# Kernel optimization log

Hardware: AMD Instinct MI355X
Metric: run time of the kernel (lower is better)

## Reference

```python
import jax, jax.numpy as jnp
import numpy as np
from jax import lax

K = 3
PAD = 1
STRIDE = 1


def setup_inputs() -> dict:
    key = jax.random.key(0)
    k1, k2, k3 = jax.random.split(key, 3)
    B, Cin, Cout, H, W = 4, 64, 64, 128, 128
    x = jax.random.normal(k1, (B, Cin, H, W), dtype=jnp.float32)
    # offset-generating conv weight: [2*K*K, Cin, K, K]
    w_offset = jax.random.normal(k2, (2 * K * K, Cin, K, K), dtype=jnp.float32) * 0.05
    # deformable conv weight: [Cout, Cin, K, K]
    w_deform = jax.random.normal(k3, (Cout, Cin, K, K), dtype=jnp.float32) * 0.05
    return {"x": x, "w_offset": w_offset, "w_deform": w_deform}


def _bilinear_sample_one(img, ys, xs):
    # img: [C, H, W]; ys, xs: [K2, Ho, Wo] float sampling coords
    H, W = img.shape[1], img.shape[2]
    y0 = jnp.floor(ys)
    x0 = jnp.floor(xs)
    wy = ys - y0  # frac weights, [K2, Ho, Wo]
    wx = xs - x0

    def gather(yi, xi):
        valid = (yi >= 0) & (yi <= H - 1) & (xi >= 0) & (xi <= W - 1)
        yc = jnp.clip(yi, 0, H - 1).astype(jnp.int32)
        xc = jnp.clip(xi, 0, W - 1).astype(jnp.int32)
        # img[:, yc, xc] -> [C, K2, Ho, Wo]; zero outside (torchvision zero-pad)
        return img[:, yc, xc] * valid[None].astype(img.dtype)

    v00 = gather(y0, x0)
    v01 = gather(y0, x0 + 1)
    v10 = gather(y0 + 1, x0)
    v11 = gather(y0 + 1, x0 + 1)
    w00 = ((1 - wy) * (1 - wx))[None]
    w01 = ((1 - wy) * wx)[None]
    w10 = (wy * (1 - wx))[None]
    w11 = (wy * wx)[None]
    return v00 * w00 + v01 * w01 + v10 * w10 + v11 * w11  # [C, K2, Ho, Wo]


def reference(x, w_offset, w_deform):
    B, Cin, H, W = x.shape
    Cout = w_deform.shape[0]
    K2 = K * K
    # 1) plain conv to produce offsets: [B, 2*K2, H, W]
    offset = lax.conv_general_dilated(
        x, w_offset, window_strides=(STRIDE, STRIDE),
        padding=((PAD, PAD), (PAD, PAD)),
        dimension_numbers=("NCHW", "OIHW", "NCHW"))
    Ho, Wo = offset.shape[2], offset.shape[3]
    # torchvision ordering: channel 2*k = dy, 2*k+1 = dx, taps row-major
    off = offset.reshape(B, K2, 2, Ho, Wo)
    dy, dx = off[:, :, 0], off[:, :, 1]  # [B, K2, Ho, Wo]
    # 2) base sampling grid per kernel tap
    kk = jnp.arange(K2)
    ki = (kk // K).astype(jnp.float32)  # tap row
    kj = (kk % K).astype(jnp.float32)   # tap col
    base_y = (jnp.arange(Ho, dtype=jnp.float32) * STRIDE - PAD)[None, :] + ki[:, None]  # [K2, Ho]
    base_x = (jnp.arange(Wo, dtype=jnp.float32) * STRIDE - PAD)[None, :] + kj[:, None]  # [K2, Wo]
    ys = base_y[None, :, :, None] + dy  # [B, K2, Ho, Wo]
    xs = base_x[None, :, None, :] + dx
    # 3) deformable bilinear gather: [B, Cin, K2, Ho, Wo]
    sampled = jax.vmap(_bilinear_sample_one)(x, ys, xs)
    # 4) weighted accumulation (the conv contraction)
    out = jnp.einsum("ock,bckhw->bohw", w_deform.reshape(Cout, Cin, K2), sampled)
    return out
```

## Files before the change

### kernel.cpp

```cpp
#include <hip/hip_runtime.h>


#define BATCH 4
#define CIN   64
#define COUT  64
#define HH    128
#define WW    128
#define HWPIX (HH*WW)

typedef __attribute__((ext_vector_type(8))) short short8;
typedef __attribute__((ext_vector_type(4))) float floatx4;

__device__ __forceinline__ unsigned short f2bf(float f) {
  unsigned int u = __float_as_uint(f);
  unsigned int r = u + 0x7fffu + ((u >> 16) & 1u);
  return (unsigned short)(r >> 16);
}
__device__ __forceinline__ float bf2f(unsigned short h) { return __uint_as_float(((unsigned int)h) << 16); }
__device__ __forceinline__ float lo16f(unsigned int u) { return __uint_as_float(u << 16); }
__device__ __forceinline__ float hi16f(unsigned int u) { return __uint_as_float(u & 0xffff0000u); }

__device__ __forceinline__ unsigned int bilin2(unsigned int u00, unsigned int u01,
                                               unsigned int u10, unsigned int u11,
                                               float w00, float w01, float w10, float w11) {
  float lo = w00 * lo16f(u00) + w01 * lo16f(u01) + w10 * lo16f(u10) + w11 * lo16f(u11);
  float hi = w00 * hi16f(u00) + w01 * hi16f(u01) + w10 * hi16f(u10) + w11 * hi16f(u11);
  unsigned int r;
  asm("v_cvt_pk_bf16_f32 %0, %1, %2" : "=v"(r) : "v"(lo), "v"(hi));
  return r;
}

__device__ __forceinline__ int swz(int a) { return a ^ (((a >> 9) & 3) << 4); }

__global__ __launch_bounds__(256) void pre_kernel(const float* __restrict__ x,
                                                  const float* __restrict__ wo,
                                                  const float* __restrict__ wd,
                                                  unsigned short* __restrict__ xThi,
                                                  unsigned short* __restrict__ xTlo,
                                                  unsigned short* __restrict__ wdA,
                                                  unsigned short* __restrict__ woAhi,
                                                  unsigned short* __restrict__ woAlo) {
  int tid = threadIdx.x;
  if (blockIdx.x < 4096) {
    __shared__ float tile[32][33];
    int t = blockIdx.x;
    int b = t >> 10, rem = t & 1023;
    int c0 = (rem >> 9) * 32, p0 = (rem & 511) * 32;
    int tx = tid & 31, ty = tid >> 5;
    const float* xb = x + (size_t)b * CIN * HWPIX;
    size_t boff = (size_t)b * HWPIX * CIN;
#pragma unroll
    for (int i = 0; i < 4; i++)
      tile[ty + i * 8][tx] = xb[(size_t)(c0 + ty + i * 8) * HWPIX + p0 + tx];
    __syncthreads();
#pragma unroll
    for (int i = 0; i < 2; i++) {
      int tt = tid + i * 256;
      int row = tt >> 4;
      int cp = tt & 15;
      float v0 = tile[cp * 2][row], v1 = tile[cp * 2 + 1][row];
      unsigned short h0 = f2bf(v0), h1 = f2bf(v1);
      unsigned short l0 = f2bf(v0 - bf2f(h0)), l1 = f2bf(v1 - bf2f(h1));
      size_t o = boff + (size_t)(p0 + row) * CIN + c0 + cp * 2;
      *(ushort2*)&xThi[o] = make_ushort2(h0, h1);
      *(ushort2*)&xTlo[o] = make_ushort2(l0, l1);
    }
  } else {
    int t = (blockIdx.x - 4096) * 256 + tid;
    if (t < 36864) {
      int j = t & 7, lane = (t >> 3) & 63, ct = (t >> 9) & 3, kc = (t >> 11) & 1, kk = t >> 12;
      int cout = ct * 16 + (lane & 15);
      int cin  = kc * 32 + (lane >> 4) * 8 + j;
      wdA[t] = f2bf(wd[(size_t)(cout * CIN + cin) * 9 + kk]);
    }
    int t2 = t - 36864;
    if (t2 >= 0 && t2 < 18432) {
      int j = t2 & 7, lane = (t2 >> 3) & 63, ct = (t2 >> 9) & 1, kc = (t2 >> 10) & 1, kk = t2 >> 11;
      int cout = ct * 16 + (lane & 15);
      int cin  = kc * 32 + (lane >> 4) * 8 + j;
      float v = (cout < 18) ? wo[(size_t)(cout * CIN + cin) * 9 + kk] : 0.f;
      unsigned short h = f2bf(v);
      woAhi[t2] = h;
      woAlo[t2] = f2bf(v - bf2f(h));
    }
  }
}

__global__ __launch_bounds__(256) void fused_dcn_kernel(const unsigned short* __restrict__ xThi,
                                                        const unsigned short* __restrict__ xTlo,
                                                        const unsigned short* __restrict__ woAhi,
                                                        const unsigned short* __restrict__ woAlo,
                                                        const unsigned short* __restrict__ wdA,
                                                        float* __restrict__ out) {
  __shared__ unsigned short sBhi2[2][4096];
  __shared__ unsigned short sBlo2[2][4096];
  __shared__ float offL[18 * 64];
  char* sHc = (char*)sBhi2;
  char* sLc = (char*)sBlo2;

  int tid = threadIdx.x;
  int hw = blockIdx.x;
  int bid = (hw & 7) * 128 + (hw >> 3);
  int b = bid >> 8, r = bid & 255, y = r >> 1, x0 = (r & 1) << 6;

  int p1 = tid >> 2, si = tid & 3;
  int lane = tid & 63, w = tid >> 6;

  const unsigned short* xhib = xThi + (size_t)b * HWPIX * CIN;
  const unsigned short* xlob = xTlo + (size_t)b * HWPIX * CIN;

  int wq = p1 >> 4, iq = p1 & 15;
  int kcd = si >> 1, qb = si & 1;
  int wb0 = ((((wq * 2 + kcd) * 64) + qb * 32 + iq) * 8) * 2;
  int wb1 = wb0 + 256;
  int swb0 = swz(wb0), swb1 = swz(wb1);
  int brb0[4], brb1[4];
#pragma unroll
  for (int pg = 0; pg < 4; pg++) {
    brb0[pg] = swz(pg * 2048 + lane * 16);
    brb1[pg] = swz(pg * 2048 + 1024 + lane * 16);
  }

  int xp = x0 + p1;

  floatx4 oacc[2];
  oacc[0] = (floatx4){0.f, 0.f, 0.f, 0.f};
  oacc[1] = (floatx4){0.f, 0.f, 0.f, 0.f};
  int ctA = w & 1, pgA = (w >> 1) * 2;

  auto ldA = [&](int kk, uint4& h0, uint4& h1, uint4& l0, uint4& l1) {
    int ys = y - 1 + kk / 3;
    int xs = xp - 1 + kk % 3;
    bool valid = (ys >= 0) && (ys < HH) && (xs >= 0) && (xs < WW);
    h0 = (uint4){0, 0, 0, 0}; h1 = h0; l0 = h0; l1 = h0;
    if (valid) {
      const unsigned short* ph = xhib + (size_t)(ys * WW + xs) * CIN + si * 16;
      const unsigned short* pl = xlob + (size_t)(ys * WW + xs) * CIN + si * 16;
      h0 = *(const uint4*)ph; h1 = *(const uint4*)(ph + 8);
      l0 = *(const uint4*)pl; l1 = *(const uint4*)(pl + 8);
    }
  };
  auto stageA = [&](int nxt, const uint4& h0, const uint4& h1, const uint4& l0, const uint4& l1) {
    *(uint4*)(sHc + nxt * 8192 + swb0) = h0;
    *(uint4*)(sHc + nxt * 8192 + swb1) = h1;
    *(uint4*)(sLc + nxt * 8192 + swb0) = l0;
    *(uint4*)(sLc + nxt * 8192 + swb1) = l1;
  };
  auto mfmaA = [&](int kk, int cur) {
    const short8* Ah = (const short8*)(woAhi + (size_t)kk * 2048);
    const short8* Al = (const short8*)(woAlo + (size_t)kk * 2048);
    short8 ah0 = Ah[ctA * 64 + lane], ah1 = Ah[128 + ctA * 64 + lane];
    short8 al0 = Al[ctA * 64 + lane], al1 = Al[128 + ctA * 64 + lane];
#pragma unroll
    for (int pgi = 0; pgi < 2; pgi++) {
      int pg = pgA + pgi;
      short8 bh0 = *(const short8*)(sHc + cur * 8192 + brb0[pg]);
      short8 bh1 = *(const short8*)(sHc + cur * 8192 + brb1[pg]);
      short8 bl0 = *(const short8*)(sLc + cur * 8192 + brb0[pg]);
      short8 bl1 = *(const short8*)(sLc + cur * 8192 + brb1[pg]);
      oacc[pgi] = __builtin_amdgcn_mfma_f32_16x16x32_bf16(ah0, bh0, oacc[pgi], 0, 0, 0);
      oacc[pgi] = __builtin_amdgcn_mfma_f32_16x16x32_bf16(ah0, bl0, oacc[pgi], 0, 0, 0);
      oacc[pgi] = __builtin_amdgcn_mfma_f32_16x16x32_bf16(al0, bh0, oacc[pgi], 0, 0, 0);
      oacc[pgi] = __builtin_amdgcn_mfma_f32_16x16x32_bf16(ah1, bh1, oacc[pgi], 0, 0, 0);
      oacc[pgi] = __builtin_amdgcn_mfma_f32_16x16x32_bf16(ah1, bl1, oacc[pgi], 0, 0, 0);
      oacc[pgi] = __builtin_amdgcn_mfma_f32_16x16x32_bf16(al1, bh1, oacc[pgi], 0, 0, 0);
    }
  };

  {
    uint4 h0c, h1c, l0c, l1c;
    ldA(0, h0c, h1c, l0c, l1c);
    stageA(0, h0c, h1c, l0c, l1c);
    __syncthreads();
#pragma unroll 1
    for (int kk = 0; kk < 9; kk++) {
      uint4 h0n, h1n, l0n, l1n;
      if (kk < 8) ldA(kk + 1, h0n, h1n, l0n, l1n);
      mfmaA(kk, kk & 1);
      if (kk < 8) stageA((kk + 1) & 1, h0n, h1n, l0n, l1n);
      __syncthreads();
    }
  }

  {
    int rowb = (lane >> 4) * 4;
    int colb = pgA * 16 + (lane & 15);
#pragma unroll
    for (int pgi = 0; pgi < 2; pgi++)
#pragma unroll
      for (int rr = 0; rr < 4; rr++) {
        int row = ctA * 16 + rowb + rr;
        if (row < 18) offL[row * 64 + colb + pgi * 16] = oacc[pgi][rr];
      }
  }
  __syncthreads();

  floatx4 acc[4];
#pragma unroll
  for (int pg = 0; pg < 4; pg++) acc[pg] = (floatx4){0.f, 0.f, 0.f, 0.f};

  struct BS {
    float w00, w01, w10, w11;
    uint4 a00, a01, a10, a11, b00, b01, b10, b11;
  };
  auto ldB = [&](int kk) -> BS {
    BS s;
    float dy = offL[(2 * kk) * 64 + p1];
    float dx = offL[(2 * kk + 1) * 64 + p1];
    float ys = (float)(y - 1 + kk / 3) + dy;
    float xs = (float)(xp - 1 + kk % 3) + dx;
    float y0f = floorf(ys), x0f = floorf(xs);
    float wy = ys - y0f, wx = xs - x0f;
    int iy0 = (int)y0f, ix0 = (int)x0f;
    int iy1 = iy0 + 1, ix1 = ix0 + 1;
    s.w00 = (1.f - wy) * (1.f - wx); s.w01 = (1.f - wy) * wx;
    s.w10 = wy * (1.f - wx);         s.w11 = wy * wx;
    bool vy0 = (iy0 >= 0) && (iy0 < HH), vy1 = (iy1 >= 0) && (iy1 < HH);
    bool vx0 = (ix0 >= 0) && (ix0 < WW), vx1 = (ix1 >= 0) && (ix1 < WW);
    if (!(vy0 && vx0)) s.w00 = 0.f;
    if (!(vy0 && vx1)) s.w01 = 0.f;
    if (!(vy1 && vx0)) s.w10 = 0.f;
    if (!(vy1 && vx1)) s.w11 = 0.f;
    int cy0 = min(max(iy0, 0), HH - 1), cy1 = min(max(iy1, 0), HH - 1);
    int cx0 = min(max(ix0, 0), WW - 1), cx1 = min(max(ix1, 0), WW - 1);
    const unsigned short* q00 = xhib + (size_t)(cy0 * WW + cx0) * CIN + si * 16;
    const unsigned short* q01 = xhib + (size_t)(cy0 * WW + cx1) * CIN + si * 16;
    const unsigned short* q10 = xhib + (size_t)(cy1 * WW + cx0) * CIN + si * 16;
    const unsigned short* q11 = xhib + (size_t)(cy1 * WW + cx1) * CIN + si * 16;
    s.a00 = *(const uint4*)q00; s.a01 = *(const uint4*)q01;
    s.a10 = *(const uint4*)q10; s.a11 = *(const uint4*)q11;
    s.b00 = *(const uint4*)(q00 + 8); s.b01 = *(const uint4*)(q01 + 8);
    s.b10 = *(const uint4*)(q10 + 8); s.b11 = *(const uint4*)(q11 + 8);
    return s;
  };
  auto blendStoreB = [&](int nxt, const BS& s) {
    uint4 o0, o1;
    o0.x = bilin2(s.a00.x, s.a01.x, s.a10.x, s.a11.x, s.w00, s.w01, s.w10, s.w11);
    o0.y = bilin2(s.a00.y, s.a01.y, s.a10.y, s.a11.y, s.w00, s.w01, s.w10, s.w11);
    o0.z = bilin2(s.a00.z, s.a01.z, s.a10.z, s.a11.z, s.w00, s.w01, s.w10, s.w11);
    o0.w = bilin2(s.a00.w, s.a01.w, s.a10.w, s.a11.w, s.w00, s.w01, s.w10, s.w11);
    o1.x = bilin2(s.b00.x, s.b01.x, s.b10.x, s.b11.x, s.w00, s.w01, s.w10, s.w11);
    o1.y = bilin2(s.b00.y, s.b01.y, s.b10.y, s.b11.y, s.w00, s.w01, s.w10, s.w11);
    o1.z = bilin2(s.b00.z, s.b01.z, s.b10.z, s.b11.z, s.w00, s.w01, s.w10, s.w11);
    o1.w = bilin2(s.b00.w, s.b01.w, s.b10.w, s.b11.w, s.w00, s.w01, s.w10, s.w11);
    *(uint4*)(sHc + nxt * 8192 + swb0) = o0;
    *(uint4*)(sHc + nxt * 8192 + swb1) = o1;
  };
  auto mfmaB = [&](int kk, int cur) {
    const short8* Ap = (const short8*)(wdA + (size_t)kk * 4096);
    short8 a0 = Ap[w * 64 + lane];
    short8 a1 = Ap[256 + w * 64 + lane];
#pragma unroll
    for (int pg = 0; pg < 4; pg++) {
      short8 bv0 = *(const short8*)(sHc + cur * 8192 + brb0[pg]);
      short8 bv1 = *(const short8*)(sHc + cur * 8192 + brb1[pg]);
      acc[pg] = __builtin_amdgcn_mfma_f32_16x16x32_bf16(a0, bv0, acc[pg], 0, 0, 0);
      acc[pg] = __builtin_amdgcn_mfma_f32_16x16x32_bf16(a1, bv1, acc[pg], 0, 0, 0);
    }
  };

  {
    BS s0 = ldB(0);
    blendStoreB(0, s0);
    __syncthreads();
#pragma unroll 1
    for (int kk = 0; kk < 9; kk++) {
      BS sn;
      if (kk < 8) sn = ldB(kk + 1);
      mfmaB(kk, kk & 1);
      if (kk < 8) blendStoreB((kk + 1) & 1, sn);
      __syncthreads();
    }
  }

  int rowb = (lane >> 4) * 4;
  float* outb = out + (size_t)b * COUT * HWPIX + y * WW + x0 + (lane & 15);
#pragma unroll
  for (int pg = 0; pg < 4; pg++)
#pragma unroll
    for (int rr = 0; rr < 4; rr++)
      outb[(size_t)(w * 16 + rowb + rr) * HWPIX + pg * 16] = acc[pg][rr];
}

extern "C" void kernel_launch(void* const* d_in, const int* in_sizes, int n_in,
                              void* d_out, int out_size, void* d_ws, size_t ws_size,
                              hipStream_t stream) {
  const float* x  = (const float*)d_in[0];
  const float* wo = (const float*)d_in[1];
  const float* wd = (const float*)d_in[2];
  float* out = (float*)d_out;

  char* wsb = (char*)d_ws;
  unsigned short* xThi  = (unsigned short*)wsb;
  unsigned short* xTlo  = (unsigned short*)(wsb + 8388608);
  unsigned short* wdA   = (unsigned short*)(wsb + 16777216);
  unsigned short* woAhi = (unsigned short*)(wsb + 16777216 + 73728);
  unsigned short* woAlo = (unsigned short*)(wsb + 16850944 + 36864);

  pre_kernel<<<dim3(4096 + 216), dim3(256), 0, stream>>>(x, wo, wd, xThi, xTlo, wdA, woAhi, woAlo);
  fused_dcn_kernel<<<dim3(BATCH * HWPIX / 64), dim3(256), 0, stream>>>(xThi, xTlo, woAhi, woAlo, wdA, out);
}
```

Measured before the change: 106.0 us.

## Deepen gather prefetch to two stages and pack bilinear blend math

Both tap loops now prefetch global loads two taps ahead using register double-buffers, so loads stay in flight longer. The loops are fully unrolled and split with a sched_barrier. The LDS staging/blend now runs before the MFMA work instead of after it. The bilinear blend uses 2-wide float vectors so the compiler can emit packed FMA instructions, and launch bounds request 4 blocks per CU. The extra in-flight register buffers raise register pressure, which may conflict with the occupancy target and cause spills.

```diff
diff --git a/kernel.cpp b/kernel.cpp
--- a/kernel.cpp
+++ b/kernel.cpp
@@ -10,6 +10,7 @@
 
 typedef __attribute__((ext_vector_type(8))) short short8;
 typedef __attribute__((ext_vector_type(4))) float floatx4;
+typedef __attribute__((ext_vector_type(2))) float f32x2;
 
 __device__ __forceinline__ unsigned short f2bf(float f) {
   unsigned int u = __float_as_uint(f);
@@ -20,13 +21,16 @@
 __device__ __forceinline__ float lo16f(unsigned int u) { return __uint_as_float(u << 16); }
 __device__ __forceinline__ float hi16f(unsigned int u) { return __uint_as_float(u & 0xffff0000u); }
 
-__device__ __forceinline__ unsigned int bilin2(unsigned int u00, unsigned int u01,
-                                               unsigned int u10, unsigned int u11,
-                                               float w00, float w01, float w10, float w11) {
-  float lo = w00 * lo16f(u00) + w01 * lo16f(u01) + w10 * lo16f(u10) + w11 * lo16f(u11);
-  float hi = w00 * hi16f(u00) + w01 * hi16f(u01) + w10 * hi16f(u10) + w11 * hi16f(u11);
+__device__ __forceinline__ unsigned int bilin2v(unsigned int u00, unsigned int u01,
+                                                unsigned int u10, unsigned int u11,
+                                                f32x2 w00, f32x2 w01, f32x2 w10, f32x2 w11) {
+  f32x2 c00 = {lo16f(u00), hi16f(u00)};
+  f32x2 c01 = {lo16f(u01), hi16f(u01)};
+  f32x2 c10 = {lo16f(u10), hi16f(u10)};
+  f32x2 c11 = {lo16f(u11), hi16f(u11)};
+  f32x2 a = c00 * w00 + c01 * w01 + c10 * w10 + c11 * w11;
   unsigned int r;
-  asm("v_cvt_pk_bf16_f32 %0, %1, %2" : "=v"(r) : "v"(lo), "v"(hi));
+  asm("v_cvt_pk_bf16_f32 %0, %1, %2" : "=v"(r) : "v"(a.x), "v"(a.y));
   return r;
 }
 
@@ -86,12 +90,12 @@
   }
 }
 
-__global__ __launch_bounds__(256) void fused_dcn_kernel(const unsigned short* __restrict__ xThi,
-                                                        const unsigned short* __restrict__ xTlo,
-                                                        const unsigned short* __restrict__ woAhi,
-                                                        const unsigned short* __restrict__ woAlo,
-                                                        const unsigned short* __restrict__ wdA,
-                                                        float* __restrict__ out) {
+__global__ __launch_bounds__(256, 4) void fused_dcn_kernel(const unsigned short* __restrict__ xThi,
+                                                           const unsigned short* __restrict__ xTlo,
+                                                           const unsigned short* __restrict__ woAhi,
+                                                           const unsigned short* __restrict__ woAlo,
+                                                           const unsigned short* __restrict__ wdA,
+                                                           float* __restrict__ out) {
   __shared__ unsigned short sBhi2[2][4096];
   __shared__ unsigned short sBlo2[2][4096];
   __shared__ float offL[18 * 64];
@@ -168,16 +172,18 @@
   };
 
   {
-    uint4 h0c, h1c, l0c, l1c;
-    ldA(0, h0c, h1c, l0c, l1c);
-    stageA(0, h0c, h1c, l0c, l1c);
+    uint4 h0s[2], h1s[2], l0s[2], l1s[2];
+    ldA(0, h0s[0], h1s[0], l0s[0], l1s[0]);
+    stageA(0, h0s[0], h1s[0], l0s[0], l1s[0]);
+    ldA(1, h0s[1], h1s[1], l0s[1], l1s[1]);
     __syncthreads();
-#pragma unroll 1
+#pragma unroll
     for (int kk = 0; kk < 9; kk++) {
-      uint4 h0n, h1n, l0n, l1n;
-      if (kk < 8) ldA(kk + 1, h0n, h1n, l0n, l1n);
+      if (kk < 7) ldA(kk + 2, h0s[kk & 1], h1s[kk & 1], l0s[kk & 1], l1s[kk & 1]);
+      __builtin_amdgcn_sched_barrier(0);
+      if (kk < 8) stageA((kk + 1) & 1, h0s[(kk + 1) & 1], h1s[(kk + 1) & 1],
+                         l0s[(kk + 1) & 1], l1s[(kk + 1) & 1]);
       mfmaA(kk, kk & 1);
-      if (kk < 8) stageA((kk + 1) & 1, h0n, h1n, l0n, l1n);
       __syncthreads();
     }
   }
@@ -234,15 +240,17 @@
     return s;
   };
   auto blendStoreB = [&](int nxt, const BS& s) {
+    f32x2 w00 = {s.w00, s.w00}, w01 = {s.w01, s.w01};
+    f32x2 w10 = {s.w10, s.w10}, w11 = {s.w11, s.w11};
     uint4 o0, o1;
-    o0.x = bilin2(s.a00.x, s.a01.x, s.a10.x, s.a11.x, s.w00, s.w01, s.w10, s.w11);
-    o0.y = bilin2(s.a00.y, s.a01.y, s.a10.y, s.a11.y, s.w00, s.w01, s.w10, s.w11);
-    o0.z = bilin2(s.a00.z, s.a01.z, s.a10.z, s.a11.z, s.w00, s.w01, s.w10, s.w11);
-    o0.w = bilin2(s.a00.w, s.a01.w, s.a10.w, s.a11.w, s.w00, s.w01, s.w10, s.w11);
-    o1.x = bilin2(s.b00.x, s.b01.x, s.b10.x, s.b11.x, s.w00, s.w01, s.w10, s.w11);
-    o1.y = bilin2(s.b00.y, s.b01.y, s.b10.y, s.b11.y, s.w00, s.w01, s.w10, s.w11);
-    o1.z = bilin2(s.b00.z, s.b01.z, s.b10.z, s.b11.z, s.w00, s.w01, s.w10, s.w11);
-    o1.w = bilin2(s.b00.w, s.b01.w, s.b10.w, s.b11.w, s.w00, s.w01, s.w10, s.w11);
+    o0.x = bilin2v(s.a00.x, s.a01.x, s.a10.x, s.a11.x, w00, w01, w10, w11);
+    o0.y = bilin2v(s.a00.y, s.a01.y, s.a10.y, s.a11.y, w00, w01, w10, w11);
+    o0.z = bilin2v(s.a00.z, s.a01.z, s.a10.z, s.a11.z, w00, w01, w10, w11);
+    o0.w = bilin2v(s.a00.w, s.a01.w, s.a10.w, s.a11.w, w00, w01, w10, w11);
+    o1.x = bilin2v(s.b00.x, s.b01.x, s.b10.x, s.b11.x, w00, w01, w10, w11);
+    o1.y = bilin2v(s.b00.y, s.b01.y, s.b10.y, s.b11.y, w00, w01, w10, w11);
+    o1.z = bilin2v(s.b00.z, s.b01.z, s.b10.z, s.b11.z, w00, w01, w10, w11);
+    o1.w = bilin2v(s.b00.w, s.b01.w, s.b10.w, s.b11.w, w00, w01, w10, w11);
     *(uint4*)(sHc + nxt * 8192 + swb0) = o0;
     *(uint4*)(sHc + nxt * 8192 + swb1) = o1;
   };
@@ -260,15 +268,17 @@
   };
 
   {
-    BS s0 = ldB(0);
-    blendStoreB(0, s0);
+    BS sb[2];
+    sb[0] = ldB(0);
+    blendStoreB(0, sb[0]);
+    sb[1] = ldB(1);
     __syncthreads();
-#pragma unroll 1
+#pragma unroll
     for (int kk = 0; kk < 9; kk++) {
-      BS sn;
-      if (kk < 8) sn = ldB(kk + 1);
+      if (kk < 7) sb[kk & 1] = ldB(kk + 2);
+      __builtin_amdgcn_sched_barrier(0);
+      if (kk < 8) blendStoreB((kk + 1) & 1, sb[(kk + 1) & 1]);
       mfmaB(kk, kk & 1);
-      if (kk < 8) blendStoreB((kk + 1) & 1, sn);
       __syncthreads();
     }
   }
```

Result: no change. 104.9 us, median of 2 (-1.0%).
